# Kernel tuning notes

Measured on AMD Instinct MI355X. Metric: run time of the kernel, lower is better.

The kernel has to match this reference:

```python
import jax, jax.numpy as jnp
import numpy as np

V, D, L, H, T = 32000, 1024, 4, 16, 1024
DH = D // H
SCALE = DH ** -0.5
FF = 4 * D
R = 2  # n_rounds


def setup_inputs() -> dict:
    key = jax.random.key(0)
    ks = iter(jax.random.split(key, 32))
    s = 0.02
    nrm = lambda shape: jax.random.normal(next(ks), shape, dtype=jnp.float32) * s
    inp = {
        "x": jax.random.randint(next(ks), (2, T), 0, V),
        "embed": nrm((V, D)),
        "pos_embed": nrm((T, D)),
        "Wqkv": nrm((L, R, 3 * D, D)),
        "bqkv": jnp.zeros((L, R, 3 * D), jnp.float32),
        "Wo": nrm((L, D, D)),
        "bo": jnp.zeros((L, D), jnp.float32),
        "Wg": nrm((L, D, 2 * D)),
        "bg": jnp.zeros((L, D), jnp.float32),
        "ln1_g": jnp.ones((L, D), jnp.float32),
        "ln1_b": jnp.zeros((L, D), jnp.float32),
        "W1": nrm((L, FF, D)),
        "b1": jnp.zeros((L, FF), jnp.float32),
        "W2": nrm((L, D, FF)),
        "b2": jnp.zeros((L, D), jnp.float32),
        "ln2_g": jnp.ones((L, D), jnp.float32),
        "ln2_b": jnp.zeros((L, D), jnp.float32),
        "lnf_g": jnp.ones((D,), jnp.float32),
        "lnf_b": jnp.zeros((D,), jnp.float32),
    }
    return inp


def _ln(h, g, b, eps=1e-5):
    m = jnp.mean(h, axis=-1, keepdims=True)
    v = jnp.mean((h - m) ** 2, axis=-1, keepdims=True)
    return (h - m) * jax.lax.rsqrt(v + eps) * g + b


def _attend(h, W, b, mask):
    B, Tq, _ = h.shape
    qkv = (h @ W.T + b).reshape(B, Tq, 3, H, DH)
    q, k, v = qkv[:, :, 0], qkv[:, :, 1], qkv[:, :, 2]  # [B,T,H,DH]
    scores = jnp.einsum("bqhd,bkhd->bhqk", q, k) * SCALE
    scores = jnp.where(mask, scores, -jnp.inf)
    a = jax.nn.softmax(scores, axis=-1)
    return jnp.einsum("bhqk,bkhd->bqhd", a, v).reshape(B, Tq, D)


def reference(x, embed, pos_embed, Wqkv, bqkv, Wo, bo, Wg, bg,
              ln1_g, ln1_b, W1, b1, W2, b2, ln2_g, ln2_b, lnf_g, lnf_b):
    B, Tq = x.shape
    mask = jnp.tril(jnp.ones((Tq, Tq), dtype=bool))
    h = embed[x] + pos_embed[jnp.arange(Tq)]
    for l in range(L):
        n1 = _ln(h, ln1_g[l], ln1_b[l])
        pred = _attend(n1, Wqkv[l, 0], bqkv[l, 0], mask)
        cum = pred
        out = pred
        # boosted round 2: attend on residual, gate the correction
        corr = _attend(n1 - cum, Wqkv[l, 1], bqkv[l, 1], mask)
        gate = jax.nn.sigmoid(jnp.concatenate([cum, corr], axis=-1) @ Wg[l].T + bg[l])
        gated = gate * corr
        out = out + gated
        h = h + (out @ Wo[l].T + bo[l])
        n2 = _ln(h, ln2_g[l], ln2_b[l])
        ff = jax.nn.gelu(n2 @ W1[l].T + b1[l], approximate=False) @ W2[l].T + b2[l]
        h = h + ff
    return _ln(h, lnf_g, lnf_b) @ embed.T  # tied head, no bias
```

## Files before the change

### kernel.cpp

```cpp
#include <hip/hip_runtime.h>
#include <math.h>

#define D_  1024
#define T_  1024
#define B_  2
#define H_  16
#define DH_ 64
#define L_  4
#define FF_ 4096
#define V_  32000
#define M_  2048

typedef _Float16 f16;
typedef _Float16 f16x8 __attribute__((ext_vector_type(8)));
typedef _Float16 f16x4 __attribute__((ext_vector_type(4)));
typedef _Float16 f16x2 __attribute__((ext_vector_type(2)));
typedef float    fx4  __attribute__((ext_vector_type(4)));

__global__ __launch_bounds__(256) void f2h_k(const float* __restrict__ in, f16* __restrict__ out) {
    const long i = ((long)blockIdx.x * 256 + threadIdx.x) * 4;
    const float4 v = *(const float4*)(in + i);
    f16x4 o = { (f16)v.x, (f16)v.y, (f16)v.z, (f16)v.w };
    *(f16x4*)(out + i) = o;
}

__global__ __launch_bounds__(256) void embed_k(const int* __restrict__ x, const float* __restrict__ emb,
                                               const float* __restrict__ pos, float* __restrict__ h) {
    const long m = blockIdx.x;
    const int  t = threadIdx.x;
    const long tok = x[m];
    const long pt  = m & (T_ - 1);
    const float4 e = ((const float4*)(emb + tok * D_))[t];
    const float4 p = ((const float4*)(pos + pt * D_))[t];
    ((float4*)(h + m * D_))[t] = make_float4(e.x + p.x, e.y + p.y, e.z + p.z, e.w + p.w);
}

__global__ __launch_bounds__(256) void ln_k(const float* __restrict__ x, const float* __restrict__ g,
                                            const float* __restrict__ b, float* __restrict__ of,
                                            f16* __restrict__ oh) {
    const long m = blockIdx.x;
    const int  t = threadIdx.x;
    const int  wave = t >> 6, lane = t & 63;
    __shared__ float red1[4], red2[4];
    const float4 v = ((const float4*)(x + m * D_))[t];
    float s = v.x + v.y + v.z + v.w;
#pragma unroll
    for (int off = 32; off; off >>= 1) s += __shfl_xor(s, off, 64);
    if (lane == 0) red1[wave] = s;
    __syncthreads();
    const float mean = (red1[0] + red1[1] + red1[2] + red1[3]) * (1.0f / 1024.0f);
    const float d0 = v.x - mean, d1 = v.y - mean, d2 = v.z - mean, d3 = v.w - mean;
    float s2 = d0 * d0 + d1 * d1 + d2 * d2 + d3 * d3;
#pragma unroll
    for (int off = 32; off; off >>= 1) s2 += __shfl_xor(s2, off, 64);
    if (lane == 0) red2[wave] = s2;
    __syncthreads();
    const float var  = (red2[0] + red2[1] + red2[2] + red2[3]) * (1.0f / 1024.0f);
    const float rstd = rsqrtf(var + 1e-5f);
    const float4 gv = ((const float4*)g)[t];
    const float4 bv = ((const float4*)b)[t];
    const float o0 = d0 * rstd * gv.x + bv.x;
    const float o1 = d1 * rstd * gv.y + bv.y;
    const float o2 = d2 * rstd * gv.z + bv.z;
    const float o3 = d3 * rstd * gv.w + bv.w;
    if (of) ((float4*)(of + m * D_))[t] = make_float4(o0, o1, o2, o3);
    if (oh) { f16x4 o = { (f16)o0, (f16)o1, (f16)o2, (f16)o3 }; *(f16x4*)(oh + m * D_ + t * 4) = o; }
}

__global__ __launch_bounds__(256) void sub_k(const float* __restrict__ a, const float* __restrict__ b,
                                             f16* __restrict__ o) {
    const long i = ((long)blockIdx.x * 256 + threadIdx.x) * 4;
    const float4 va = *(const float4*)(a + i);
    const float4 vb = *(const float4*)(b + i);
    f16x4 o4 = { (f16)(va.x - vb.x), (f16)(va.y - vb.y), (f16)(va.z - vb.z), (f16)(va.w - vb.w) };
    *(f16x4*)(o + i) = o4;
}

__global__ __launch_bounds__(256) void cat_k(const float* __restrict__ p, const float* __restrict__ c,
                                             f16* __restrict__ o) {
    const long i = ((long)blockIdx.x * 256 + threadIdx.x) * 4;
    const long m = i >> 11;
    const int  j = (int)(i & 2047);
    const float* src = (j < 1024) ? (p + m * 1024 + j) : (c + m * 1024 + (j - 1024));
    const float4 v = *(const float4*)src;
    f16x4 o4 = { (f16)v.x, (f16)v.y, (f16)v.z, (f16)v.w };
    *(f16x4*)(o + i) = o4;
}

__global__ __launch_bounds__(256) void gate_k(const float* __restrict__ p, const float* __restrict__ c,
                                              const float* __restrict__ gl, f16* __restrict__ o) {
    const long i = ((long)blockIdx.x * 256 + threadIdx.x) * 4;
    const float4 vp = *(const float4*)(p + i);
    const float4 vc = *(const float4*)(c + i);
    const float4 vg = *(const float4*)(gl + i);
    const float s0 = 1.0f / (1.0f + __expf(-vg.x));
    const float s1 = 1.0f / (1.0f + __expf(-vg.y));
    const float s2 = 1.0f / (1.0f + __expf(-vg.z));
    const float s3 = 1.0f / (1.0f + __expf(-vg.w));
    f16x4 o4 = { (f16)(vp.x + s0 * vc.x), (f16)(vp.y + s1 * vc.y),
                 (f16)(vp.z + s2 * vc.z), (f16)(vp.w + s3 * vc.w) };
    *(f16x4*)(o + i) = o4;
}

template<int BN>
__global__ __launch_bounds__(256)
void gemm_bt(const f16* __restrict__ A, const f16* __restrict__ Wt,
             const float* __restrict__ bias, const float* __restrict__ resid,
             float* __restrict__ Cf, f16* __restrict__ Ch,
             int N, int K, int gelu) {
    __shared__ __align__(16) f16 As[3][128 * 32];
    __shared__ __align__(16) f16 Bs[3][BN * 32];
    const int tid  = threadIdx.x;
    const int wave = tid >> 6;
    const int lane = tid & 63;

    const int nbm = gridDim.y;
    const int nbn = gridDim.x;
    int bi = blockIdx.y * nbn + blockIdx.x;
    const int nwg = nbm * nbn;
    if ((nwg & 7) == 0) bi = (bi & 7) * (nwg >> 3) + (bi >> 3);
    const long bm = bi % nbm;
    const long bn = bi / nbm;

    const int wm = (wave >> 1) * 64;
    const int wn = (wave & 1) * (BN / 2);
    constexpr int NJ = BN / 32;

    fx4 acc[4][NJ] = {};

    const int c0 = wave * 2;
    const int r0 = c0 * 16 + (lane >> 2);
    const int cc = ((lane & 3) ^ ((lane >> 3) & 3)) * 8;
    const f16* a0 = A + ((long)bm * 128 + r0) * K + cc;
    const f16* a1 = A + ((long)bm * 128 + r0 + 16) * K + cc;

    const f16* b0;
    const f16* b1 = nullptr;
    if constexpr (BN == 128) {
        b0 = Wt + ((long)bn * 128 + r0) * K + cc;
        b1 = Wt + ((long)bn * 128 + r0 + 16) * K + cc;
    } else {
        b0 = Wt + ((long)bn * 64 + wave * 16 + (lane >> 2)) * K + cc;
    }

    const int NT = K >> 5;

    auto STAGE = [&](int kt) {
        const int k0 = kt * 32;
        const int bf3 = kt % 3;
        __builtin_amdgcn_global_load_lds((const __attribute__((address_space(1))) void*)(a0 + k0),
                                         (__attribute__((address_space(3))) void*)&As[bf3][c0 * 512], 16, 0, 0);
        __builtin_amdgcn_global_load_lds((const __attribute__((address_space(1))) void*)(a1 + k0),
                                         (__attribute__((address_space(3))) void*)&As[bf3][(c0 + 1) * 512], 16, 0, 0);
        if constexpr (BN == 128) {
            __builtin_amdgcn_global_load_lds((const __attribute__((address_space(1))) void*)(b0 + k0),
                                             (__attribute__((address_space(3))) void*)&Bs[bf3][c0 * 512], 16, 0, 0);
            __builtin_amdgcn_global_load_lds((const __attribute__((address_space(1))) void*)(b1 + k0),
                                             (__attribute__((address_space(3))) void*)&Bs[bf3][(c0 + 1) * 512], 16, 0, 0);
        } else {
            __builtin_amdgcn_global_load_lds((const __attribute__((address_space(1))) void*)(b0 + k0),
                                             (__attribute__((address_space(3))) void*)&Bs[bf3][wave * 512], 16, 0, 0);
        }
    };

    STAGE(0);
    if (NT > 1) STAGE(1);

    const int lm = lane & 15;
    const int g  = lane >> 4;
    const int koff = (g ^ ((lm >> 1) & 3)) * 8;
    for (int t = 0; t < NT; ++t) {
        if (t + 2 < NT) STAGE(t + 2);
        const int rem = NT - 1 - t;
        if constexpr (BN == 128) {
            if (rem >= 2)      asm volatile("s_waitcnt vmcnt(8)" ::: "memory");
            else if (rem == 1) asm volatile("s_waitcnt vmcnt(4)" ::: "memory");
            else               asm volatile("s_waitcnt vmcnt(0)" ::: "memory");
        } else {
            if (rem >= 2)      asm volatile("s_waitcnt vmcnt(6)" ::: "memory");
            else if (rem == 1) asm volatile("s_waitcnt vmcnt(3)" ::: "memory");
            else               asm volatile("s_waitcnt vmcnt(0)" ::: "memory");
        }
        __builtin_amdgcn_s_barrier();
        __builtin_amdgcn_sched_barrier(0);

        const f16* as = As[t % 3];
        const f16* bs = Bs[t % 3];
        f16x8 af[4], bf[NJ];
#pragma unroll
        for (int i = 0; i < 4; ++i)
            af[i] = *(const f16x8*)&as[(wm + i * 16 + lm) * 32 + koff];
#pragma unroll
        for (int j = 0; j < NJ; ++j)
            bf[j] = *(const f16x8*)&bs[(wn + j * 16 + lm) * 32 + koff];
#pragma unroll
        for (int i = 0; i < 4; ++i)
#pragma unroll
            for (int j = 0; j < NJ; ++j)
                acc[i][j] = __builtin_amdgcn_mfma_f32_16x16x32_f16(af[i], bf[j], acc[i][j], 0, 0, 0);

        asm volatile("s_waitcnt lgkmcnt(0)" ::: "memory");
        __builtin_amdgcn_sched_barrier(0);
        __builtin_amdgcn_s_barrier();
    }

    float* esc = (float*)&As[0][0] + (size_t)wave * 320;
    const int erow = lane >> 2;
    const int ecg  = (lane & 3) * 4;
    const long gr0 = bm * 128 + wm;
    const long gc0 = bn * BN + wn;
#pragma unroll
    for (int i = 0; i < 4; ++i) {
#pragma unroll
        for (int j = 0; j < NJ; ++j) {
#pragma unroll
            for (int r = 0; r < 4; ++r)
                esc[(g * 4 + r) * 20 + lm] = acc[i][j][r];
            asm volatile("s_waitcnt lgkmcnt(0)" ::: "memory");
            __builtin_amdgcn_sched_barrier(0);
            const fx4 q = *(const fx4*)&esc[erow * 20 + ecg];
            asm volatile("s_waitcnt lgkmcnt(0)" ::: "memory");
            __builtin_amdgcn_sched_barrier(0);
            const long row = gr0 + i * 16 + erow;
            const long col = gc0 + j * 16 + ecg;
            fx4 v = q;
            if (bias) {
                const fx4 b4 = *(const fx4*)&bias[col];
                v[0] += b4[0]; v[1] += b4[1]; v[2] += b4[2]; v[3] += b4[3];
            }
            if (gelu) {
#pragma unroll
                for (int e = 0; e < 4; ++e)
                    v[e] = 0.5f * v[e] * (1.0f + erff(v[e] * 0.70710678118654752f));
            } else if (resid) {
                const fx4 rz = *(const fx4*)&resid[row * (long)N + col];
                v[0] += rz[0]; v[1] += rz[1]; v[2] += rz[2]; v[3] += rz[3];
            }
            if (Cf) *(fx4*)&Cf[row * (long)N + col] = v;
            if (Ch) {
                f16x4 hq = { (f16)v[0], (f16)v[1], (f16)v[2], (f16)v[3] };
                *(f16x4*)&Ch[row * (long)N + col] = hq;
            }
        }
    }
}

__global__ __launch_bounds__(256) void fattn_k(const f16* __restrict__ qkv, float* __restrict__ out) {
    __shared__ __align__(16) f16 Ks[128 * 72];
    __shared__ __align__(16) f16 Vt[64 * 136];
    __shared__ __align__(16) f16 Pw[4][16 * 136];
    const int tid  = threadIdx.x;
    const int w    = tid >> 6;
    const int lane = tid & 63;
    const int b  = blockIdx.z, h = blockIdx.y;
    const int qt = (gridDim.x - 1) - blockIdx.x;
    const int q0w = qt * 64 + w * 16;
    const int g  = lane >> 4;
    const int lm = lane & 15;

    const long qrow = ((long)(b * T_ + q0w + lm)) * (3 * D_) + h * DH_;
    f16x8 af_q[2];
    af_q[0] = *(const f16x8*)(qkv + qrow + g * 8);
    af_q[1] = *(const f16x8*)(qkv + qrow + 32 + g * 8);

    float m_r[4], l_r[4];
    fx4 acc_o[4] = {};
#pragma unroll
    for (int r = 0; r < 4; ++r) { m_r[r] = -INFINITY; l_r[r] = 0.0f; }

    const int krow = tid >> 1;
    const int kdh  = (tid & 1) * 32;
    const long kbase = ((long)(b * T_)) * (3 * D_) + D_ + h * DH_ + kdh;
    const int vm  = tid >> 2;
    const int vd0 = (tid & 3) * 16;
    const long vbase = ((long)(b * T_)) * (3 * D_) + 2 * D_ + h * DH_ + vd0;

    const int nit = (qt >> 1) + 1;

    f16x8 kr0, kr1, kr2, kr3, vr0, vr1, vr2, vr3;
    {
        const f16* ks = qkv + kbase + (long)krow * (3 * D_);
        kr0 = *(const f16x8*)(ks);
        kr1 = *(const f16x8*)(ks + 8);
        kr2 = *(const f16x8*)(ks + 16);
        kr3 = *(const f16x8*)(ks + 24);
        const f16* va = qkv + vbase + (long)(2 * vm) * (3 * D_);
        vr0 = *(const f16x8*)(va);
        vr1 = *(const f16x8*)(va + 8);
        vr2 = *(const f16x8*)(va + 3 * D_);
        vr3 = *(const f16x8*)(va + 3 * D_ + 8);
    }

    for (int it = 0; it < nit; ++it) {
        const int kb = it * 128;
        __syncthreads();
        *(f16x8*)&Ks[krow * 72 + kdh]      = kr0;
        *(f16x8*)&Ks[krow * 72 + kdh + 8]  = kr1;
        *(f16x8*)&Ks[krow * 72 + kdh + 16] = kr2;
        *(f16x8*)&Ks[krow * 72 + kdh + 24] = kr3;
#pragma unroll
        for (int jj = 0; jj < 16; ++jj) {
            const int d = vd0 + jj;
            const f16 va_ = (jj < 8) ? vr0[jj] : vr1[jj - 8];
            const f16 vb_ = (jj < 8) ? vr2[jj] : vr3[jj - 8];
            const int col = (2 * vm) ^ (((d >> 2) & 7) << 3);
            f16x2 pr = { va_, vb_ };
            *(f16x2*)&Vt[d * 136 + col] = pr;
        }
        __syncthreads();

        if (it + 1 < nit) {
            const int kb2 = kb + 128;
            const f16* ks = qkv + kbase + (long)(kb2 + krow) * (3 * D_);
            kr0 = *(const f16x8*)(ks);
            kr1 = *(const f16x8*)(ks + 8);
            kr2 = *(const f16x8*)(ks + 16);
            kr3 = *(const f16x8*)(ks + 24);
            const f16* va = qkv + vbase + (long)(kb2 + 2 * vm) * (3 * D_);
            vr0 = *(const f16x8*)(va);
            vr1 = *(const f16x8*)(va + 8);
            vr2 = *(const f16x8*)(va + 3 * D_);
            vr3 = *(const f16x8*)(va + 3 * D_ + 8);
        }

        const int qmax = q0w + 15;
        int nact = qmax - kb + 1; if (nact > 128) nact = 128;
        const int nkt = (nact + 15) >> 4;
        const int nkc = (nact + 31) >> 5;
        const bool diag = (kb + 127 > q0w);

        fx4 sc[8];
#pragma unroll
        for (int kt = 0; kt < 8; ++kt) {
            if (kt < nkt) {
                fx4 c = {};
#pragma unroll
                for (int kk = 0; kk < 2; ++kk) {
                    f16x8 bf = *(const f16x8*)&Ks[(kt * 16 + lm) * 72 + kk * 32 + g * 8];
                    c = __builtin_amdgcn_mfma_f32_16x16x32_f16(af_q[kk], bf, c, 0, 0, 0);
                }
                c *= 0.125f;
                if (diag) {
                    const int key_g = kb + kt * 16 + lm;
#pragma unroll
                    for (int r = 0; r < 4; ++r)
                        if (key_g > q0w + g * 4 + r) c[r] = -INFINITY;
                }
                sc[kt] = c;
            }
        }

        float mnew[4], pscale[4];
#pragma unroll
        for (int r = 0; r < 4; ++r) {
            float tm = -INFINITY;
#pragma unroll
            for (int kt = 0; kt < 8; ++kt)
                if (kt < nkt) tm = fmaxf(tm, sc[kt][r]);
#pragma unroll
            for (int off = 8; off; off >>= 1) tm = fmaxf(tm, __shfl_xor(tm, off, 64));
            mnew[r]   = fmaxf(m_r[r], tm);
            pscale[r] = __expf(m_r[r] - mnew[r]);
        }
        float psum[4] = {};
#pragma unroll
        for (int kt = 0; kt < 8; ++kt) {
            if (kt < nkt) {
#pragma unroll
                for (int r = 0; r < 4; ++r) {
                    const float p = __expf(sc[kt][r] - mnew[r]);
                    sc[kt][r] = p;
                    psum[r] += p;
                }
            }
        }
#pragma unroll
        for (int r = 0; r < 4; ++r) {
#pragma unroll
            for (int off = 8; off; off >>= 1) psum[r] += __shfl_xor(psum[r], off, 64);
            l_r[r] = l_r[r] * pscale[r] + psum[r];
            m_r[r] = mnew[r];
        }
#pragma unroll
        for (int nt = 0; nt < 4; ++nt)
#pragma unroll
            for (int r = 0; r < 4; ++r) acc_o[nt][r] *= pscale[r];

        f16* P = Pw[w];
#pragma unroll
        for (int kt = 0; kt < 8; ++kt) {
            if (kt < nkt) {
#pragma unroll
                for (int r = 0; r < 4; ++r)
                    P[(g * 4 + r) * 136 + kt * 16 + lm] = (f16)sc[kt][r];
            } else if (kt == nkt) {
#pragma unroll
                for (int r = 0; r < 4; ++r)
                    P[(g * 4 + r) * 136 + kt * 16 + lm] = (f16)0.0f;
            }
        }

#pragma unroll
        for (int kc = 0; kc < 4; ++kc) {
            if (kc < nkc) {
                f16x8 ap = *(const f16x8*)&P[lm * 136 + kc * 32 + g * 8];
#pragma unroll
                for (int nt = 0; nt < 4; ++nt) {
                    const int d = nt * 16 + lm;
                    const int col = (kc * 32 + g * 8) ^ (((d >> 2) & 7) << 3);
                    f16x8 bv = *(const f16x8*)&Vt[d * 136 + col];
                    acc_o[nt] = __builtin_amdgcn_mfma_f32_16x16x32_f16(ap, bv, acc_o[nt], 0, 0, 0);
                }
            }
        }
    }

    const long obase = ((long)(b * T_ + q0w + g * 4)) * D_ + h * DH_ + lm;
#pragma unroll
    for (int r = 0; r < 4; ++r) {
        const float inv = 1.0f / l_r[r];
#pragma unroll
        for (int nt = 0; nt < 4; ++nt)
            out[obase + (long)r * D_ + nt * 16] = acc_o[nt][r] * inv;
    }
}

extern "C" void kernel_launch(void* const* d_in, const int* in_sizes, int n_in,
                              void* d_out, int out_size, void* d_ws, size_t ws_size,
                              hipStream_t stream) {
    const int*   x    = (const int*)d_in[0];
    const float* emb  = (const float*)d_in[1];
    const float* pos  = (const float*)d_in[2];
    const float* Wqkv = (const float*)d_in[3];
    const float* bqkv = (const float*)d_in[4];
    const float* Wo   = (const float*)d_in[5];
    const float* bo   = (const float*)d_in[6];
    const float* Wg   = (const float*)d_in[7];
    const float* bg   = (const float*)d_in[8];
    const float* ln1g = (const float*)d_in[9];
    const float* ln1b = (const float*)d_in[10];
    const float* W1   = (const float*)d_in[11];
    const float* b1   = (const float*)d_in[12];
    const float* W2   = (const float*)d_in[13];
    const float* b2   = (const float*)d_in[14];
    const float* ln2g = (const float*)d_in[15];
    const float* ln2b = (const float*)d_in[16];
    const float* lnfg = (const float*)d_in[17];
    const float* lnfb = (const float*)d_in[18];
    float* out = (float*)d_out;

    char* ws = (char*)d_ws;
    size_t off = 0;
    auto alloc = [&](size_t bytes) -> void* {
        off = (off + 255) & ~(size_t)255;
        void* p = ws + off;
        off += bytes;
        return p;
    };
    float* h    = (float*)alloc((size_t)M_ * D_ * 4);
    float* n1f  = (float*)alloc((size_t)M_ * D_ * 4);
    float* pred = (float*)alloc((size_t)M_ * D_ * 4);
    float* corr = (float*)alloc((size_t)M_ * D_ * 4);
    float* glin = (float*)alloc((size_t)M_ * D_ * 4);
    f16* qkvh  = (f16*)alloc((size_t)M_ * 3 * D_ * 2);
    f16* ab    = (f16*)alloc((size_t)M_ * D_ * 2);
    f16* catb  = (f16*)alloc((size_t)M_ * 2 * D_ * 2);
    f16* ffh   = (f16*)alloc((size_t)M_ * FF_ * 2);
    f16* embh  = (f16*)alloc((size_t)V_ * D_ * 2);
    f16* wqkvh = (f16*)alloc((size_t)L_ * 2 * 3 * D_ * D_ * 2);
    f16* woh   = (f16*)alloc((size_t)L_ * D_ * D_ * 2);
    f16* wgh   = (f16*)alloc((size_t)L_ * D_ * 2 * D_ * 2);
    f16* w1h   = (f16*)alloc((size_t)L_ * FF_ * D_ * 2);
    f16* w2h   = (f16*)alloc((size_t)L_ * D_ * FF_ * 2);

    auto cvt = [&](const float* src, f16* dst, long n) {
        f2h_k<<<dim3((unsigned)(n / 1024)), dim3(256), 0, stream>>>(src, dst);
    };
    cvt(emb,  embh,  (long)V_ * D_);
    cvt(Wqkv, wqkvh, (long)L_ * 2 * 3 * D_ * D_);
    cvt(Wo,   woh,   (long)L_ * D_ * D_);
    cvt(Wg,   wgh,   (long)L_ * D_ * 2 * D_);
    cvt(W1,   w1h,   (long)L_ * FF_ * D_);
    cvt(W2,   w2h,   (long)L_ * D_ * FF_);

    embed_k<<<dim3(M_), dim3(256), 0, stream>>>(x, emb, pos, h);

    auto gemm = [&](const f16* A, const f16* Wt, const float* bias, const float* resid,
                    float* Cf, f16* Ch, int N, int K, int gelu) {
        if (N <= 1024)
            gemm_bt<64><<<dim3(N / 64, M_ / 128), dim3(256), 0, stream>>>(A, Wt, bias, resid, Cf, Ch, N, K, gelu);
        else
            gemm_bt<128><<<dim3(N / 128, M_ / 128), dim3(256), 0, stream>>>(A, Wt, bias, resid, Cf, Ch, N, K, gelu);
    };

    for (int l = 0; l < L_; ++l) {
        ln_k<<<dim3(M_), 256, 0, stream>>>(h, ln1g + l * D_, ln1b + l * D_, n1f, ab);
        gemm(ab, wqkvh + (size_t)(l * 2 + 0) * 3 * D_ * D_, bqkv + (l * 2 + 0) * 3 * D_,
             nullptr, nullptr, qkvh, 3 * D_, D_, 0);
        fattn_k<<<dim3(T_ / 64, H_, B_), 256, 0, stream>>>(qkvh, pred);
        sub_k<<<dim3(M_ * D_ / 1024), 256, 0, stream>>>(n1f, pred, ab);
        gemm(ab, wqkvh + (size_t)(l * 2 + 1) * 3 * D_ * D_, bqkv + (l * 2 + 1) * 3 * D_,
             nullptr, nullptr, qkvh, 3 * D_, D_, 0);
        fattn_k<<<dim3(T_ / 64, H_, B_), 256, 0, stream>>>(qkvh, corr);
        cat_k<<<dim3(M_ * 2 * D_ / 1024), 256, 0, stream>>>(pred, corr, catb);
        gemm(catb, wgh + (size_t)l * D_ * 2 * D_, bg + l * D_, nullptr, glin, nullptr, D_, 2 * D_, 0);
        gate_k<<<dim3(M_ * D_ / 1024), 256, 0, stream>>>(pred, corr, glin, ab);
        gemm(ab, woh + (size_t)l * D_ * D_, bo + l * D_, h, h, nullptr, D_, D_, 0);
        ln_k<<<dim3(M_), 256, 0, stream>>>(h, ln2g + l * D_, ln2b + l * D_, nullptr, ab);
        gemm(ab, w1h + (size_t)l * FF_ * D_, b1 + l * FF_, nullptr, nullptr, ffh, FF_, D_, 1);
        gemm(ffh, w2h + (size_t)l * D_ * FF_, b2 + l * D_, h, h, nullptr, D_, FF_, 0);
    }
    ln_k<<<dim3(M_), 256, 0, stream>>>(h, lnfg, lnfb, nullptr, ab);
    gemm(ab, embh, nullptr, nullptr, out, nullptr, V_, D_, 0);
}
```

Before: 2.149 ms.

## Fuse residual subtraction into attention and gating into gate GEMM; double-buffer GEMM

Removes the separate sub_k and gate_k elementwise kernels. The n1-minus-pred f16 residual is now written in the attention epilogue, and the sigmoid gate plus pred + gate*corr is computed in the gate GEMM epilogue, which writes f16 directly and drops the glin buffer. The GEMM pipeline also shrinks from triple to double buffering in LDS, with matching waitcnt changes. That frees LDS and may raise occupancy, but leaves less room to hide load latency.

```diff
diff --git a/kernel.cpp b/kernel.cpp
--- a/kernel.cpp
+++ b/kernel.cpp
@@ -67,15 +67,6 @@
     if (oh) { f16x4 o = { (f16)o0, (f16)o1, (f16)o2, (f16)o3 }; *(f16x4*)(oh + m * D_ + t * 4) = o; }
 }
 
-__global__ __launch_bounds__(256) void sub_k(const float* __restrict__ a, const float* __restrict__ b,
-                                             f16* __restrict__ o) {
-    const long i = ((long)blockIdx.x * 256 + threadIdx.x) * 4;
-    const float4 va = *(const float4*)(a + i);
-    const float4 vb = *(const float4*)(b + i);
-    f16x4 o4 = { (f16)(va.x - vb.x), (f16)(va.y - vb.y), (f16)(va.z - vb.z), (f16)(va.w - vb.w) };
-    *(f16x4*)(o + i) = o4;
-}
-
 __global__ __launch_bounds__(256) void cat_k(const float* __restrict__ p, const float* __restrict__ c,
                                              f16* __restrict__ o) {
     const long i = ((long)blockIdx.x * 256 + threadIdx.x) * 4;
@@ -87,29 +78,15 @@
     *(f16x4*)(o + i) = o4;
 }
 
-__global__ __launch_bounds__(256) void gate_k(const float* __restrict__ p, const float* __restrict__ c,
-                                              const float* __restrict__ gl, f16* __restrict__ o) {
-    const long i = ((long)blockIdx.x * 256 + threadIdx.x) * 4;
-    const float4 vp = *(const float4*)(p + i);
-    const float4 vc = *(const float4*)(c + i);
-    const float4 vg = *(const float4*)(gl + i);
-    const float s0 = 1.0f / (1.0f + __expf(-vg.x));
-    const float s1 = 1.0f / (1.0f + __expf(-vg.y));
-    const float s2 = 1.0f / (1.0f + __expf(-vg.z));
-    const float s3 = 1.0f / (1.0f + __expf(-vg.w));
-    f16x4 o4 = { (f16)(vp.x + s0 * vc.x), (f16)(vp.y + s1 * vc.y),
-                 (f16)(vp.z + s2 * vc.z), (f16)(vp.w + s3 * vc.w) };
-    *(f16x4*)(o + i) = o4;
-}
-
 template<int BN>
 __global__ __launch_bounds__(256)
 void gemm_bt(const f16* __restrict__ A, const f16* __restrict__ Wt,
              const float* __restrict__ bias, const float* __restrict__ resid,
+             const float* __restrict__ gate_corr,
              float* __restrict__ Cf, f16* __restrict__ Ch,
              int N, int K, int gelu) {
-    __shared__ __align__(16) f16 As[3][128 * 32];
-    __shared__ __align__(16) f16 Bs[3][BN * 32];
+    __shared__ __align__(16) f16 As[2][128 * 32];
+    __shared__ __align__(16) f16 Bs[2][BN * 32];
     const int tid  = threadIdx.x;
     const int wave = tid >> 6;
     const int lane = tid & 63;
@@ -147,45 +124,42 @@
 
     auto STAGE = [&](int kt) {
         const int k0 = kt * 32;
-        const int bf3 = kt % 3;
+        const int bf2 = kt & 1;
         __builtin_amdgcn_global_load_lds((const __attribute__((address_space(1))) void*)(a0 + k0),
-                                         (__attribute__((address_space(3))) void*)&As[bf3][c0 * 512], 16, 0, 0);
+                                         (__attribute__((address_space(3))) void*)&As[bf2][c0 * 512], 16, 0, 0);
         __builtin_amdgcn_global_load_lds((const __attribute__((address_space(1))) void*)(a1 + k0),
-                                         (__attribute__((address_space(3))) void*)&As[bf3][(c0 + 1) * 512], 16, 0, 0);
+                                         (__attribute__((address_space(3))) void*)&As[bf2][(c0 + 1) * 512], 16, 0, 0);
         if constexpr (BN == 128) {
             __builtin_amdgcn_global_load_lds((const __attribute__((address_space(1))) void*)(b0 + k0),
-                                             (__attribute__((address_space(3))) void*)&Bs[bf3][c0 * 512], 16, 0, 0);
+                                             (__attribute__((address_space(3))) void*)&Bs[bf2][c0 * 512], 16, 0, 0);
             __builtin_amdgcn_global_load_lds((const __attribute__((address_space(1))) void*)(b1 + k0),
-                                             (__attribute__((address_space(3))) void*)&Bs[bf3][(c0 + 1) * 512], 16, 0, 0);
+                                             (__attribute__((address_space(3))) void*)&Bs[bf2][(c0 + 1) * 512], 16, 0, 0);
         } else {
             __builtin_amdgcn_global_load_lds((const __attribute__((address_space(1))) void*)(b0 + k0),
-                                             (__attribute__((address_space(3))) void*)&Bs[bf3][wave * 512], 16, 0, 0);
+                                             (__attribute__((address_space(3))) void*)&Bs[bf2][wave * 512], 16, 0, 0);
         }
     };
 
     STAGE(0);
-    if (NT > 1) STAGE(1);
 
     const int lm = lane & 15;
     const int g  = lane >> 4;
     const int koff = (g ^ ((lm >> 1) & 3)) * 8;
     for (int t = 0; t < NT; ++t) {
-        if (t + 2 < NT) STAGE(t + 2);
-        const int rem = NT - 1 - t;
+        const bool more = (t + 1 < NT);
+        if (more) STAGE(t + 1);
         if constexpr (BN == 128) {
-            if (rem >= 2)      asm volatile("s_waitcnt vmcnt(8)" ::: "memory");
-            else if (rem == 1) asm volatile("s_waitcnt vmcnt(4)" ::: "memory");
-            else               asm volatile("s_waitcnt vmcnt(0)" ::: "memory");
+            if (more) asm volatile("s_waitcnt vmcnt(4)" ::: "memory");
+            else      asm volatile("s_waitcnt vmcnt(0)" ::: "memory");
         } else {
-            if (rem >= 2)      asm volatile("s_waitcnt vmcnt(6)" ::: "memory");
-            else if (rem == 1) asm volatile("s_waitcnt vmcnt(3)" ::: "memory");
-            else               asm volatile("s_waitcnt vmcnt(0)" ::: "memory");
+            if (more) asm volatile("s_waitcnt vmcnt(3)" ::: "memory");
+            else      asm volatile("s_waitcnt vmcnt(0)" ::: "memory");
         }
         __builtin_amdgcn_s_barrier();
         __builtin_amdgcn_sched_barrier(0);
 
-        const f16* as = As[t % 3];
-        const f16* bs = Bs[t % 3];
+        const f16* as = As[t & 1];
+        const f16* bs = Bs[t & 1];
         f16x8 af[4], bf[NJ];
 #pragma unroll
         for (int i = 0; i < 4; ++i)
@@ -228,6 +202,18 @@
                 const fx4 b4 = *(const fx4*)&bias[col];
                 v[0] += b4[0]; v[1] += b4[1]; v[2] += b4[2]; v[3] += b4[3];
             }
+            if (gate_corr) {
+                const fx4 pz = *(const fx4*)&resid[row * (long)N + col];
+                const fx4 cz = *(const fx4*)&gate_corr[row * (long)N + col];
+#pragma unroll
+                for (int e = 0; e < 4; ++e) {
+                    const float s = 1.0f / (1.0f + __expf(-v[e]));
+                    v[e] = pz[e] + s * cz[e];
+                }
+                f16x4 hq = { (f16)v[0], (f16)v[1], (f16)v[2], (f16)v[3] };
+                *(f16x4*)&Ch[row * (long)N + col] = hq;
+                continue;
+            }
             if (gelu) {
 #pragma unroll
                 for (int e = 0; e < 4; ++e)
@@ -245,7 +231,8 @@
     }
 }
 
-__global__ __launch_bounds__(256) void fattn_k(const f16* __restrict__ qkv, float* __restrict__ out) {
+__global__ __launch_bounds__(256) void fattn_k(const f16* __restrict__ qkv, float* __restrict__ out,
+                                               const float* __restrict__ n1, f16* __restrict__ dif) {
     __shared__ __align__(16) f16 Ks[128 * 72];
     __shared__ __align__(16) f16 Vt[64 * 136];
     __shared__ __align__(16) f16 Pw[4][16 * 136];
@@ -420,8 +407,12 @@
     for (int r = 0; r < 4; ++r) {
         const float inv = 1.0f / l_r[r];
 #pragma unroll
-        for (int nt = 0; nt < 4; ++nt)
-            out[obase + (long)r * D_ + nt * 16] = acc_o[nt][r] * inv;
+        for (int nt = 0; nt < 4; ++nt) {
+            const long idx = obase + (long)r * D_ + nt * 16;
+            const float val = acc_o[nt][r] * inv;
+            out[idx] = val;
+            if (dif) dif[idx] = (f16)(n1[idx] - val);
+        }
     }
 }
 
@@ -461,7 +452,6 @@
     float* n1f  = (float*)alloc((size_t)M_ * D_ * 4);
     float* pred = (float*)alloc((size_t)M_ * D_ * 4);
     float* corr = (float*)alloc((size_t)M_ * D_ * 4);
-    float* glin = (float*)alloc((size_t)M_ * D_ * 4);
     f16* qkvh  = (f16*)alloc((size_t)M_ * 3 * D_ * 2);
     f16* ab    = (f16*)alloc((size_t)M_ * D_ * 2);
     f16* catb  = (f16*)alloc((size_t)M_ * 2 * D_ * 2);
@@ -486,30 +476,28 @@
     embed_k<<<dim3(M_), dim3(256), 0, stream>>>(x, emb, pos, h);
 
     auto gemm = [&](const f16* A, const f16* Wt, const float* bias, const float* resid,
-                    float* Cf, f16* Ch, int N, int K, int gelu) {
+                    const float* gate_corr, float* Cf, f16* Ch, int N, int K, int gelu) {
         if (N <= 1024)
-            gemm_bt<64><<<dim3(N / 64, M_ / 128), dim3(256), 0, stream>>>(A, Wt, bias, resid, Cf, Ch, N, K, gelu);
+            gemm_bt<64><<<dim3(N / 64, M_ / 128), dim3(256), 0, stream>>>(A, Wt, bias, resid, gate_corr, Cf, Ch, N, K, gelu);
         else
-            gemm_bt<128><<<dim3(N / 128, M_ / 128), dim3(256), 0, stream>>>(A, Wt, bias, resid, Cf, Ch, N, K, gelu);
+            gemm_bt<128><<<dim3(N / 128, M_ / 128), dim3(256), 0, stream>>>(A, Wt, bias, resid, gate_corr, Cf, Ch, N, K, gelu);
     };
 
     for (int l = 0; l < L_; ++l) {
         ln_k<<<dim3(M_), 256, 0, stream>>>(h, ln1g + l * D_, ln1b + l * D_, n1f, ab);
         gemm(ab, wqkvh + (size_t)(l * 2 + 0) * 3 * D_ * D_, bqkv + (l * 2 + 0) * 3 * D_,
-             nullptr, nullptr, qkvh, 3 * D_, D_, 0);
-        fattn_k<<<dim3(T_ / 64, H_, B_), 256, 0, stream>>>(qkvh, pred);
-        sub_k<<<dim3(M_ * D_ / 1024), 256, 0, stream>>>(n1f, pred, ab);
+             nullptr, nullptr, nullptr, qkvh, 3 * D_, D_, 0);
+        fattn_k<<<dim3(T_ / 64, H_, B_), 256, 0, stream>>>(qkvh, pred, n1f, ab);
         gemm(ab, wqkvh + (size_t)(l * 2 + 1) * 3 * D_ * D_, bqkv + (l * 2 + 1) * 3 * D_,
-             nullptr, nullptr, qkvh, 3 * D_, D_, 0);
-        fattn_k<<<dim3(T_ / 64, H_, B_), 256, 0, stream>>>(qkvh, corr);
+             nullptr, nullptr, nullptr, qkvh, 3 * D_, D_, 0);
+        fattn_k<<<dim3(T_ / 64, H_, B_), 256, 0, stream>>>(qkvh, corr, nullptr, nullptr);
         cat_k<<<dim3(M_ * 2 * D_ / 1024), 256, 0, stream>>>(pred, corr, catb);
-        gemm(catb, wgh + (size_t)l * D_ * 2 * D_, bg + l * D_, nullptr, glin, nullptr, D_, 2 * D_, 0);
-        gate_k<<<dim3(M_ * D_ / 1024), 256, 0, stream>>>(pred, corr, glin, ab);
-        gemm(ab, woh + (size_t)l * D_ * D_, bo + l * D_, h, h, nullptr, D_, D_, 0);
+        gemm(catb, wgh + (size_t)l * D_ * 2 * D_, bg + l * D_, pred, corr, nullptr, ab, D_, 2 * D_, 0);
+        gemm(ab, woh + (size_t)l * D_ * D_, bo + l * D_, h, nullptr, h, nullptr, D_, D_, 0);
         ln_k<<<dim3(M_), 256, 0, stream>>>(h, ln2g + l * D_, ln2b + l * D_, nullptr, ab);
-        gemm(ab, w1h + (size_t)l * FF_ * D_, b1 + l * FF_, nullptr, nullptr, ffh, FF_, D_, 1);
-        gemm(ffh, w2h + (size_t)l * D_ * FF_, b2 + l * D_, h, h, nullptr, D_, FF_, 0);
+        gemm(ab, w1h + (size_t)l * FF_ * D_, b1 + l * FF_, nullptr, nullptr, nullptr, ffh, FF_, D_, 1);
+        gemm(ffh, w2h + (size_t)l * D_ * FF_, b2 + l * D_, h, nullptr, h, nullptr, D_, FF_, 0);
     }
     ln_k<<<dim3(M_), 256, 0, stream>>>(h, lnfg, lnfb, nullptr, ab);
-    gemm(ab, embh, nullptr, nullptr, out, nullptr, V_, D_, 0);
-}
+    gemm(ab, embh, nullptr, nullptr, nullptr, out, nullptr, V_, D_, 0);
+}
```

Measured after the change: 2.110 ms. Within noise of the previous version (-1.8%).
